# Kernel tuning notes

Measured on AMD Instinct MI355X. Metric: run time of the kernel, lower is better.

## Reference

```python
import jax, jax.numpy as jnp
import numpy as np

B, D_IN, H, OUT = 65536, 3072, 100, 10
CUTOFF = 0.5


def setup_inputs() -> dict:
    key = jax.random.key(0)
    ks = jax.random.split(key, 7)
    x = jax.random.normal(ks[0], (B, D_IN), jnp.float32)
    # Kaiming-ish scaling so activations stay sane through 15 relu layers
    w_in = jax.random.normal(ks[1], (D_IN, H), jnp.float32) * np.float32(1.0 / np.sqrt(D_IN))
    b_in = jax.random.normal(ks[2], (H,), jnp.float32) * np.float32(0.01)
    w_hid = jax.random.normal(ks[3], (14, H, H), jnp.float32) * np.float32(1.0 / np.sqrt(H))
    b_hid = jax.random.normal(ks[4], (14, H), jnp.float32) * np.float32(0.01)
    w_out = jax.random.normal(ks[5], (3, H, OUT), jnp.float32) * np.float32(1.0 / np.sqrt(H))
    b_out = jax.random.normal(ks[6], (3, OUT), jnp.float32) * np.float32(0.01)
    return {"x": x, "w_in": w_in, "b_in": b_in, "w_hid": w_hid, "b_hid": b_hid, "w_out": w_out, "b_out": b_out}


def reference(x, w_in, b_in, w_hid, b_hid, w_out, b_out):
    # Stage 0 (net0): first layer D_IN->H then 4 hidden layers H->H, all relu
    h = jax.nn.relu(x @ w_in + b_in)
    for i in range(0, 4):
        h = jax.nn.relu(h @ w_hid[i] + b_hid[i])
    out0 = h @ w_out[0] + b_out[0]                     # [B, 10]
    conf0 = jnp.max(out0, axis=1) > CUTOFF             # cutoff_mask

    # Stage 1 (net1): 5 hidden layers H->H on net0's hidden features
    for i in range(4, 9):
        h = jax.nn.relu(h @ w_hid[i] + b_hid[i])
    out1 = h @ w_out[1] + b_out[1]
    conf1 = jnp.max(out1, axis=1) > CUTOFF

    # Stage 2 (net2): 5 hidden layers H->H, output registered unconditionally
    for i in range(9, 14):
        h = jax.nn.relu(h @ w_hid[i] + b_hid[i])
    out2 = h @ w_out[2] + b_out[2]

    # Filter/reordered_output: each sample takes the output of the first stage
    # at which it was confident (early-exit cascade, dense-masked equivalent).
    final = jnp.where(conf0[:, None], out0, jnp.where(conf1[:, None], out1, out2))
    return final
```

## Files before the change

kernel.cpp:

```cpp
#include <hip/hip_runtime.h>


typedef __fp16 h2   __attribute__((ext_vector_type(2)));
typedef __fp16 h8v  __attribute__((ext_vector_type(8)));
typedef float  f4v  __attribute__((ext_vector_type(4)));
typedef float  f16v __attribute__((ext_vector_type(16)));

#define CHUNK 16384

static constexpr unsigned OFF_W1  = 0;
static constexpr unsigned OFF_WH  = 96u * CHUNK;
static constexpr unsigned OFF_WO  = OFF_WH + 56u * CHUNK;
static constexpr unsigned OFF_BIN = OFF_WO + 3u * CHUNK;
static constexpr unsigned OFF_H1  = OFF_BIN + 512;

__device__ __forceinline__ unsigned bc2(h2 v) { return __builtin_bit_cast(unsigned, v); }

__device__ __forceinline__ f4v ntld4(const float* p) {
  return __builtin_nontemporal_load((const f4v*)p);
}

__device__ __forceinline__ void lds_cp16(const char* g, char* l) {
  __builtin_amdgcn_global_load_lds(
      (const __attribute__((address_space(1))) void*)g,
      (__attribute__((address_space(3))) void*)l, 16, 0, 0);
}

__device__ __forceinline__ void stage1(const char* g, char* l, int tid) {
  lds_cp16(g + tid * 16, l + tid * 16);
}
__device__ __forceinline__ void stage2(const char* g, char* l, int tid) {
  lds_cp16(g + tid * 16, l + tid * 16);
  lds_cp16(g + 8192 + tid * 16, l + 8192 + tid * 16);
}

__device__ __forceinline__ void cvt8(f4v a, f4v b, h8v& hi, h8v& lo) {
  h2 h0 = __builtin_amdgcn_cvt_pkrtz(a[0], a[1]);
  h2 h1 = __builtin_amdgcn_cvt_pkrtz(a[2], a[3]);
  h2 h2_ = __builtin_amdgcn_cvt_pkrtz(b[0], b[1]);
  h2 h3 = __builtin_amdgcn_cvt_pkrtz(b[2], b[3]);
  h2 l0 = __builtin_amdgcn_cvt_pkrtz(a[0] - (float)h0[0], a[1] - (float)h0[1]);
  h2 l1 = __builtin_amdgcn_cvt_pkrtz(a[2] - (float)h1[0], a[3] - (float)h1[1]);
  h2 l2 = __builtin_amdgcn_cvt_pkrtz(b[0] - (float)h2_[0], b[1] - (float)h2_[1]);
  h2 l3 = __builtin_amdgcn_cvt_pkrtz(b[2] - (float)h3[0], b[3] - (float)h3[1]);
  hi = h8v{h0[0], h0[1], h1[0], h1[1], h2_[0], h2_[1], h3[0], h3[1]};
  lo = h8v{l0[0], l0[1], l1[0], l1[1], l2[0], l2[1], l3[0], l3[1]};
}

__device__ __forceinline__ void split4s(f4v v, uint2& hi, uint2& lo) {
  h2 a = __builtin_amdgcn_cvt_pkrtz(v[0], v[1]);
  h2 b = __builtin_amdgcn_cvt_pkrtz(v[2], v[3]);
  h2 c = __builtin_amdgcn_cvt_pkrtz(v[0] - (float)a[0], v[1] - (float)a[1]);
  h2 d = __builtin_amdgcn_cvt_pkrtz(v[2] - (float)b[0], v[3] - (float)b[1]);
  hi = make_uint2(bc2(a), bc2(b));
  lo = make_uint2(bc2(c), bc2(d));
}

__device__ __forceinline__ void split8w(const float* f, uint4& hi, uint4& lo) {
  h2 h0 = __builtin_amdgcn_cvt_pkrtz(f[0], f[1]);
  h2 h1 = __builtin_amdgcn_cvt_pkrtz(f[2], f[3]);
  h2 h2_ = __builtin_amdgcn_cvt_pkrtz(f[4], f[5]);
  h2 h3 = __builtin_amdgcn_cvt_pkrtz(f[6], f[7]);
  h2 l0 = __builtin_amdgcn_cvt_pkrtz(f[0] - (float)h0[0], f[1] - (float)h0[1]);
  h2 l1 = __builtin_amdgcn_cvt_pkrtz(f[2] - (float)h1[0], f[3] - (float)h1[1]);
  h2 l2 = __builtin_amdgcn_cvt_pkrtz(f[4] - (float)h2_[0], f[5] - (float)h2_[1]);
  h2 l3 = __builtin_amdgcn_cvt_pkrtz(f[6] - (float)h3[0], f[7] - (float)h3[1]);
  hi = make_uint4(bc2(h0), bc2(h1), bc2(h2_), bc2(h3));
  lo = make_uint4(bc2(l0), bc2(l1), bc2(l2), bc2(l3));
}

__device__ __forceinline__ unsigned item_off(int it) {
  if (it >= 58) return OFF_WO + 2u * CHUNK;
  if (it == 16) return OFF_WO;
  if (it == 37) return OFF_WO + CHUNK;
  int j = it - (it > 16 ? 1 : 0) - (it > 37 ? 1 : 0);
  return OFF_WH + (unsigned)j * CHUNK;
}

__global__ __launch_bounds__(256) void prep_k(
    const float* __restrict__ w_in, const float* __restrict__ b_in,
    const float* __restrict__ w_hid, const float* __restrict__ b_hid,
    const float* __restrict__ w_out, const float* __restrict__ b_out,
    char* __restrict__ ws) {
  int idx = blockIdx.x * 256 + threadIdx.x;
  int lane = idx & 63;
  int grp = idx >> 6;
  float f[8];
  uint4 hi, lo;
  if (grp < 768) {
    int mf = grp & 7, c = grp >> 3;
    int feat = mf * 16 + (lane & 15);
    int g = lane >> 4;
    int kb = c * 32 + g * 4;
#pragma unroll
    for (int e = 0; e < 8; ++e) {
      int k = kb + (e < 4 ? e : 12 + e);
      f[e] = (feat < 100) ? w_in[(size_t)k * 100 + feat] : 0.f;
    }
    split8w(f, hi, lo);
    char* dst = ws + OFF_W1 + (size_t)c * CHUNK + (size_t)mf * 2048 + lane * 16;
    *(uint4*)dst = hi;
    *(uint4*)(dst + 1024) = lo;
    return;
  }
  grp -= 768;
  if (grp < 448) {
    int j = grp & 1, ft = (grp >> 1) & 3, ch = grp >> 3;
    int L = ch >> 2, s = ch & 3;
    int feat = ft * 32 + (lane & 31);
    int k0 = s * 32 + j * 16 + (lane >> 5) * 8;
#pragma unroll
    for (int e = 0; e < 8; ++e) {
      int k = k0 + e;
      float v;
      if (k < 100 && feat < 100)  v = w_hid[(size_t)L * 10000 + k * 100 + feat];
      else if (k == 127)          v = (feat < 100) ? b_hid[L * 100 + feat]
                                                   : (feat == 127 ? 1.f : 0.f);
      else                        v = 0.f;
      f[e] = v;
    }
    split8w(f, hi, lo);
    char* dst = ws + OFF_WH + (size_t)ch * CHUNK + (size_t)((ft * 2 + j) * 2) * 1024 + lane * 16;
    *(uint4*)dst = hi;
    *(uint4*)(dst + 1024) = lo;
    return;
  }
  grp -= 448;
  if (grp < 24) {
    int kb = grp & 7, st = grp >> 3;
    int cls = lane & 31;
    int k0 = kb * 16 + (lane >> 5) * 8;
#pragma unroll
    for (int e = 0; e < 8; ++e) {
      int k = k0 + e;
      float v;
      if (cls < 10 && k < 100) v = w_out[(size_t)st * 1000 + k * 10 + cls];
      else if (k == 127)       v = (cls < 10) ? b_out[st * 10 + cls] : -60000.f;
      else                     v = 0.f;
      f[e] = v;
    }
    split8w(f, hi, lo);
    char* dst = ws + OFF_WO + (size_t)st * CHUNK + (size_t)(kb * 2) * 1024 + lane * 16;
    *(uint4*)dst = hi;
    *(uint4*)(dst + 1024) = lo;
    return;
  }
  grp -= 24;
  if (grp < 2) {
    int i = grp * 64 + lane;
    ((float*)(ws + OFF_BIN))[i] = (i < 100) ? b_in[i] : (i == 127 ? 1.f : 0.f);
  }
}

#define P1_SMEM (3 * CHUNK)

__global__ __launch_bounds__(1024, 4) void p1_k(const float* __restrict__ x,
                                                char* __restrict__ ws) {
  extern __shared__ __align__(16) char sm[];
  const int tid = threadIdx.x;
  const int lane = tid & 63, wid = tid >> 6;
  const int l15 = lane & 15, g = lane >> 4;
  const int tile = blockIdx.x;
  const char* w1g = ws + OFF_W1;
  const float* xr = x + (size_t)(tile * 256 + wid * 16 + l15) * 3072;

  f4v xP[2], xQ[2], xR[2];
  stage1(w1g, sm, tid);
  __builtin_amdgcn_sched_barrier(0);
  xP[0] = ntld4(xr + g * 4);      xP[1] = ntld4(xr + 16 + g * 4);
  __builtin_amdgcn_sched_barrier(0);
  stage1(w1g + CHUNK, sm + CHUNK, tid);
  __builtin_amdgcn_sched_barrier(0);
  xQ[0] = ntld4(xr + 32 + g * 4); xQ[1] = ntld4(xr + 48 + g * 4);
  __builtin_amdgcn_sched_barrier(0);
  xR[0] = ntld4(xr + 64 + g * 4); xR[1] = ntld4(xr + 80 + g * 4);
  __builtin_amdgcn_sched_barrier(0);

  f4v acc[8] = {};
  const int abase = lane * 16;

  auto step = [&](int s, f4v (&xa)[2]) {
    if (s <= 93)      asm volatile("s_waitcnt vmcnt(5)" ::: "memory");
    else if (s == 94) asm volatile("s_waitcnt vmcnt(3)" ::: "memory");
    else              asm volatile("s_waitcnt vmcnt(0)" ::: "memory");
    __builtin_amdgcn_s_barrier();
    asm volatile("" ::: "memory");

    h8v bhi, blo;
    cvt8(xa[0], xa[1], bhi, blo);
    if (s + 2 < 96) stage1(w1g + (size_t)(s + 2) * CHUNK, sm + ((s + 2) % 3) * CHUNK, tid);
    __builtin_amdgcn_sched_barrier(0);
    if (s + 3 < 96) {
      const int o = (s + 3) * 32 + g * 4;
      xa[0] = ntld4(xr + o); xa[1] = ntld4(xr + o + 16);
    }
    __builtin_amdgcn_sched_barrier(0);

    const char* ab = sm + (s % 3) * CHUNK + abase;
#pragma unroll
    for (int mf = 0; mf < 8; ++mf) {
      h8v ahi = *(const h8v*)(ab + mf * 2048);
      h8v alo = *(const h8v*)(ab + mf * 2048 + 1024);
      acc[mf] = __builtin_amdgcn_mfma_f32_16x16x32_f16(ahi, bhi, acc[mf], 0, 0, 0);
      acc[mf] = __builtin_amdgcn_mfma_f32_16x16x32_f16(ahi, blo, acc[mf], 0, 0, 0);
      acc[mf] = __builtin_amdgcn_mfma_f32_16x16x32_f16(alo, bhi, acc[mf], 0, 0, 0);
    }
  };

#pragma unroll 1
  for (int s3 = 0; s3 < 96; s3 += 3) {
    step(s3, xP);
    step(s3 + 1, xQ);
    step(s3 + 2, xR);
  }

  const float* bp = (const float*)(ws + OFF_BIN);
  const int p2tile = tile * 2 + (wid >> 3);
  const int rt = (wid >> 1) & 3;
  const int l31 = (wid & 1) * 16 + l15;
  char* hb = ws + OFF_H1 + (size_t)p2tile * 65536;
#pragma unroll
  for (int mf = 0; mf < 8; ++mf) {
    f4v bi = *(const f4v*)(bp + mf * 16 + g * 4);
    f4v v = acc[mf] + bi;
    v[0] = fmaxf(v[0], 0.f); v[1] = fmaxf(v[1], 0.f);
    v[2] = fmaxf(v[2], 0.f); v[3] = fmaxf(v[3], 0.f);
    uint2 hi, lo;
    split4s(v, hi, lo);
    char* dst = hb + (size_t)(rt * 8 + mf) * 2048 + (g >> 1) * 512 + l31 * 16 + (g & 1) * 8;
    *(uint2*)dst = hi;
    *(uint2*)(dst + 1024) = lo;
  }
}

#define P2_SMEM (65536 + 3 * CHUNK)

__global__ __launch_bounds__(512, 2) void p2_k(char* __restrict__ ws,
                                               float* __restrict__ out) {
  extern __shared__ __align__(16) char sm[];
  char* hsm = sm;
  char* wsm = sm + 65536;
  const int tid = threadIdx.x;
  const int lane = tid & 63, wid = tid >> 6;
  const int mr = wid & 1, rt = wid >> 1;
  const int l31 = lane & 31, gg = lane >> 5;
  const int tile = blockIdx.x;

  {
    const char* hg = ws + OFF_H1 + (size_t)tile * 65536;
#pragma unroll
    for (int i = 0; i < 8; ++i)
      lds_cp16(hg + i * 8192 + tid * 16, hsm + i * 8192 + tid * 16);
    __builtin_amdgcn_sched_barrier(0);
    stage2(ws + item_off(0), wsm, tid);
    stage2(ws + item_off(1), wsm + CHUNK, tid);
  }

  const f16v z16 = {};
  f16v a0 = {}, a1 = {};
  float s0[6], s1[6], s2[6];
  bool c0 = false, c1 = false;

  auto ring_top = [&](int i) {
    asm volatile("s_waitcnt vmcnt(2)" ::: "memory");
    __builtin_amdgcn_s_barrier();
    asm volatile("" ::: "memory");
    stage2(ws + item_off(i + 2), wsm + ((i + 2) % 3) * CHUNK, tid);
  };

  auto hidden = [&](int base) {
#pragma unroll
    for (int ss = 0; ss < 4; ++ss) {
      ring_top(base + ss);
      const char* wb = wsm + ((base + ss) % 3) * CHUNK + lane * 16;
      const char* hbp = hsm + rt * 16384 + ss * 4096 + lane * 16;
      h8v bh0 = *(const h8v*)(hbp);
      h8v bl0 = *(const h8v*)(hbp + 1024);
      h8v bh1 = *(const h8v*)(hbp + 2048);
      h8v bl1 = *(const h8v*)(hbp + 3072);
      const char* ab0 = wb + (mr * 2) * 4096;
      const char* ab1 = ab0 + 4096;
      h8v ah, al;
      ah = *(const h8v*)(ab0);        al = *(const h8v*)(ab0 + 1024);
      a0 = __builtin_amdgcn_mfma_f32_32x32x16_f16(ah, bh0, a0, 0, 0, 0);
      a0 = __builtin_amdgcn_mfma_f32_32x32x16_f16(ah, bl0, a0, 0, 0, 0);
      a0 = __builtin_amdgcn_mfma_f32_32x32x16_f16(al, bh0, a0, 0, 0, 0);
      ah = *(const h8v*)(ab0 + 2048); al = *(const h8v*)(ab0 + 3072);
      a0 = __builtin_amdgcn_mfma_f32_32x32x16_f16(ah, bh1, a0, 0, 0, 0);
      a0 = __builtin_amdgcn_mfma_f32_32x32x16_f16(ah, bl1, a0, 0, 0, 0);
      a0 = __builtin_amdgcn_mfma_f32_32x32x16_f16(al, bh1, a0, 0, 0, 0);
      ah = *(const h8v*)(ab1);        al = *(const h8v*)(ab1 + 1024);
      a1 = __builtin_amdgcn_mfma_f32_32x32x16_f16(ah, bh0, a1, 0, 0, 0);
      a1 = __builtin_amdgcn_mfma_f32_32x32x16_f16(ah, bl0, a1, 0, 0, 0);
      a1 = __builtin_amdgcn_mfma_f32_32x32x16_f16(al, bh0, a1, 0, 0, 0);
      ah = *(const h8v*)(ab1 + 2048); al = *(const h8v*)(ab1 + 3072);
      a1 = __builtin_amdgcn_mfma_f32_32x32x16_f16(ah, bh1, a1, 0, 0, 0);
      a1 = __builtin_amdgcn_mfma_f32_32x32x16_f16(ah, bl1, a1, 0, 0, 0);
      a1 = __builtin_amdgcn_mfma_f32_32x32x16_f16(al, bh1, a1, 0, 0, 0);
    }
    __builtin_amdgcn_s_barrier();
    asm volatile("" ::: "memory");
#pragma unroll
    for (int fi = 0; fi < 2; ++fi) {
      const int ftb = mr * 2 + fi;
#pragma unroll
      for (int q = 0; q < 4; ++q) {
        f4v v = fi ? f4v{a1[4 * q], a1[4 * q + 1], a1[4 * q + 2], a1[4 * q + 3]}
                   : f4v{a0[4 * q], a0[4 * q + 1], a0[4 * q + 2], a0[4 * q + 3]};
        v[0] = fmaxf(v[0], 0.f); v[1] = fmaxf(v[1], 0.f);
        v[2] = fmaxf(v[2], 0.f); v[3] = fmaxf(v[3], 0.f);
        uint2 hi, lo;
        split4s(v, hi, lo);
        const int kblk = ftb * 2 + (q >> 1);
        char* dst = hsm + (size_t)((rt * 8 + kblk) * 2) * 1024 + ((q & 1) * 32 + l31) * 16 + gg * 8;
        *(uint2*)dst = hi;
        *(uint2*)(dst + 1024) = lo;
      }
    }
    asm volatile("s_waitcnt lgkmcnt(0)" ::: "memory");
    __builtin_amdgcn_s_barrier();
    asm volatile("" ::: "memory");
    a0 = z16;
    a1 = z16;
  };

  auto wstage = [&](int i, float (&sv)[6], bool* cb) {
    ring_top(i);
    const char* wb = wsm + (i % 3) * CHUNK + lane * 16;
    if (mr == 0) {
      f16v oa = {};
#pragma unroll
      for (int kb = 0; kb < 8; ++kb) {
        h8v ah = *(const h8v*)(wb + kb * 2048);
        h8v al = *(const h8v*)(wb + kb * 2048 + 1024);
        const char* hbp = hsm + rt * 16384 + kb * 2048 + lane * 16;
        h8v bh = *(const h8v*)(hbp);
        h8v bl = *(const h8v*)(hbp + 1024);
        oa = __builtin_amdgcn_mfma_f32_32x32x16_f16(ah, bh, oa, 0, 0, 0);
        oa = __builtin_amdgcn_mfma_f32_32x32x16_f16(ah, bl, oa, 0, 0, 0);
        oa = __builtin_amdgcn_mfma_f32_32x32x16_f16(al, bh, oa, 0, 0, 0);
      }
      float m = oa[0];
#pragma unroll
      for (int r = 1; r < 16; ++r) m = fmaxf(m, oa[r]);
      m = fmaxf(m, __shfl_xor(m, 32, 64));
      if (cb) *cb = (m > 0.5f);
      sv[0] = oa[0]; sv[1] = oa[1]; sv[2] = oa[2];
      sv[3] = oa[3]; sv[4] = oa[4]; sv[5] = oa[5];
    }
  };

  hidden(0); hidden(4); hidden(8); hidden(12);
  wstage(16, s0, &c0);
  hidden(17); hidden(21); hidden(25); hidden(29); hidden(33);
  wstage(37, s1, &c1);
  hidden(38); hidden(42); hidden(46); hidden(50); hidden(54);
  wstage(58, s2, nullptr);

  if (mr == 0) {
    float r[6];
#pragma unroll
    for (int j = 0; j < 6; ++j) r[j] = c0 ? s0[j] : (c1 ? s1[j] : s2[j]);
    float* dp = out + (size_t)(tile * 128 + rt * 32 + l31) * 10;
    if (gg == 0) {
      *(float2*)(dp)     = make_float2(r[0], r[1]);
      *(float2*)(dp + 2) = make_float2(r[2], r[3]);
      *(float2*)(dp + 8) = make_float2(r[4], r[5]);
    } else {
      *(float2*)(dp + 4) = make_float2(r[0], r[1]);
      *(float2*)(dp + 6) = make_float2(r[2], r[3]);
    }
  }
}

extern "C" void kernel_launch(void* const* d_in, const int* in_sizes, int n_in,
                              void* d_out, int out_size, void* d_ws, size_t ws_size,
                              hipStream_t stream) {
  (void)in_sizes; (void)n_in; (void)out_size; (void)ws_size;
  const float* x     = (const float*)d_in[0];
  const float* w_in  = (const float*)d_in[1];
  const float* b_in  = (const float*)d_in[2];
  const float* w_hid = (const float*)d_in[3];
  const float* b_hid = (const float*)d_in[4];
  const float* w_out = (const float*)d_in[5];
  const float* b_out = (const float*)d_in[6];
  float* out = (float*)d_out;
  char* ws = (char*)d_ws;

  (void)hipFuncSetAttribute((const void*)p1_k,
                            hipFuncAttributeMaxDynamicSharedMemorySize, P1_SMEM);
  (void)hipFuncSetAttribute((const void*)p2_k,
                            hipFuncAttributeMaxDynamicSharedMemorySize, P2_SMEM);

  prep_k<<<311, 256, 0, stream>>>(w_in, b_in, w_hid, b_hid, w_out, b_out, ws);
  p1_k<<<256, 1024, P1_SMEM, stream>>>(x, ws);
  p2_k<<<512, 512, P2_SMEM, stream>>>(ws, out);
}
```

Baseline: 307.4 us.

## Double K-step size in first-layer GEMM and deepen hidden-layer weight ring to four

```diff
diff --git a/kernel.cpp b/kernel.cpp
--- a/kernel.cpp
+++ b/kernel.cpp
@@ -26,8 +26,9 @@
       (__attribute__((address_space(3))) void*)l, 16, 0, 0);
 }
 
-__device__ __forceinline__ void stage1(const char* g, char* l, int tid) {
+__device__ __forceinline__ void stageW(const char* g, char* l, int tid) {
   lds_cp16(g + tid * 16, l + tid * 16);
+  lds_cp16(g + 16384 + tid * 16, l + 16384 + tid * 16);
 }
 __device__ __forceinline__ void stage2(const char* g, char* l, int tid) {
   lds_cp16(g + tid * 16, l + tid * 16);
@@ -152,7 +153,7 @@
   }
 }
 
-#define P1_SMEM (3 * CHUNK)
+#define P1_SMEM (3 * 32768)
 
 __global__ __launch_bounds__(1024, 4) void p1_k(const float* __restrict__ x,
                                                 char* __restrict__ ws) {
@@ -164,54 +165,67 @@
   const char* w1g = ws + OFF_W1;
   const float* xr = x + (size_t)(tile * 256 + wid * 16 + l15) * 3072;
 
-  f4v xP[2], xQ[2], xR[2];
-  stage1(w1g, sm, tid);
+  f4v xP[4], xQ[4];
+  stageW(w1g, sm, tid);
   __builtin_amdgcn_sched_barrier(0);
-  xP[0] = ntld4(xr + g * 4);      xP[1] = ntld4(xr + 16 + g * 4);
+  {
+    const int o = g * 4;
+    xP[0] = ntld4(xr + o);      xP[1] = ntld4(xr + o + 16);
+    xP[2] = ntld4(xr + o + 32); xP[3] = ntld4(xr + o + 48);
+  }
   __builtin_amdgcn_sched_barrier(0);
-  stage1(w1g + CHUNK, sm + CHUNK, tid);
+  stageW(w1g + 2 * CHUNK, sm + 32768, tid);
   __builtin_amdgcn_sched_barrier(0);
-  xQ[0] = ntld4(xr + 32 + g * 4); xQ[1] = ntld4(xr + 48 + g * 4);
-  __builtin_amdgcn_sched_barrier(0);
-  xR[0] = ntld4(xr + 64 + g * 4); xR[1] = ntld4(xr + 80 + g * 4);
+  {
+    const int o = 64 + g * 4;
+    xQ[0] = ntld4(xr + o);      xQ[1] = ntld4(xr + o + 16);
+    xQ[2] = ntld4(xr + o + 32); xQ[3] = ntld4(xr + o + 48);
+  }
   __builtin_amdgcn_sched_barrier(0);
 
   f4v acc[8] = {};
   const int abase = lane * 16;
 
-  auto step = [&](int s, f4v (&xa)[2]) {
-    if (s <= 93)      asm volatile("s_waitcnt vmcnt(5)" ::: "memory");
-    else if (s == 94) asm volatile("s_waitcnt vmcnt(3)" ::: "memory");
-    else              asm volatile("s_waitcnt vmcnt(0)" ::: "memory");
+  auto step = [&](int s, f4v (&xa)[4]) {
+    if (s == 47) asm volatile("s_waitcnt vmcnt(0)" ::: "memory");
+    else         asm volatile("s_waitcnt vmcnt(6)" ::: "memory");
     __builtin_amdgcn_s_barrier();
     asm volatile("" ::: "memory");
 
-    h8v bhi, blo;
-    cvt8(xa[0], xa[1], bhi, blo);
-    if (s + 2 < 96) stage1(w1g + (size_t)(s + 2) * CHUNK, sm + ((s + 2) % 3) * CHUNK, tid);
+    h8v bh0, bl0, bh1, bl1;
+    cvt8(xa[0], xa[1], bh0, bl0);
+    cvt8(xa[2], xa[3], bh1, bl1);
+    if (s + 2 < 48) {
+      stageW(w1g + (size_t)(2 * s + 4) * CHUNK, sm + ((s + 2) % 3) * 32768, tid);
+    }
     __builtin_amdgcn_sched_barrier(0);
-    if (s + 3 < 96) {
-      const int o = (s + 3) * 32 + g * 4;
-      xa[0] = ntld4(xr + o); xa[1] = ntld4(xr + o + 16);
+    if (s + 2 < 48) {
+      const int o = (s + 2) * 64 + g * 4;
+      xa[0] = ntld4(xr + o);      xa[1] = ntld4(xr + o + 16);
+      xa[2] = ntld4(xr + o + 32); xa[3] = ntld4(xr + o + 48);
     }
     __builtin_amdgcn_sched_barrier(0);
 
-    const char* ab = sm + (s % 3) * CHUNK + abase;
+    const char* ab = sm + (s % 3) * 32768 + abase;
 #pragma unroll
     for (int mf = 0; mf < 8; ++mf) {
       h8v ahi = *(const h8v*)(ab + mf * 2048);
       h8v alo = *(const h8v*)(ab + mf * 2048 + 1024);
-      acc[mf] = __builtin_amdgcn_mfma_f32_16x16x32_f16(ahi, bhi, acc[mf], 0, 0, 0);
-      acc[mf] = __builtin_amdgcn_mfma_f32_16x16x32_f16(ahi, blo, acc[mf], 0, 0, 0);
-      acc[mf] = __builtin_amdgcn_mfma_f32_16x16x32_f16(alo, bhi, acc[mf], 0, 0, 0);
+      acc[mf] = __builtin_amdgcn_mfma_f32_16x16x32_f16(ahi, bh0, acc[mf], 0, 0, 0);
+      acc[mf] = __builtin_amdgcn_mfma_f32_16x16x32_f16(ahi, bl0, acc[mf], 0, 0, 0);
+      acc[mf] = __builtin_amdgcn_mfma_f32_16x16x32_f16(alo, bh0, acc[mf], 0, 0, 0);
+      h8v ahiB = *(const h8v*)(ab + 16384 + mf * 2048);
+      h8v aloB = *(const h8v*)(ab + 16384 + mf * 2048 + 1024);
+      acc[mf] = __builtin_amdgcn_mfma_f32_16x16x32_f16(ahiB, bh1, acc[mf], 0, 0, 0);
+      acc[mf] = __builtin_amdgcn_mfma_f32_16x16x32_f16(ahiB, bl1, acc[mf], 0, 0, 0);
+      acc[mf] = __builtin_amdgcn_mfma_f32_16x16x32_f16(aloB, bh1, acc[mf], 0, 0, 0);
     }
   };
 
 #pragma unroll 1
-  for (int s3 = 0; s3 < 96; s3 += 3) {
-    step(s3, xP);
-    step(s3 + 1, xQ);
-    step(s3 + 2, xR);
+  for (int s2 = 0; s2 < 48; s2 += 2) {
+    step(s2, xP);
+    step(s2 + 1, xQ);
   }
 
   const float* bp = (const float*)(ws + OFF_BIN);
@@ -233,7 +247,7 @@
   }
 }
 
-#define P2_SMEM (65536 + 3 * CHUNK)
+#define P2_SMEM (65536 + 4 * CHUNK)
 
 __global__ __launch_bounds__(512, 2) void p2_k(char* __restrict__ ws,
                                                float* __restrict__ out) {
@@ -254,6 +268,7 @@
     __builtin_amdgcn_sched_barrier(0);
     stage2(ws + item_off(0), wsm, tid);
     stage2(ws + item_off(1), wsm + CHUNK, tid);
+    stage2(ws + item_off(2), wsm + 2 * CHUNK, tid);
   }
 
   const f16v z16 = {};
@@ -262,17 +277,17 @@
   bool c0 = false, c1 = false;
 
   auto ring_top = [&](int i) {
-    asm volatile("s_waitcnt vmcnt(2)" ::: "memory");
+    asm volatile("s_waitcnt vmcnt(4)" ::: "memory");
     __builtin_amdgcn_s_barrier();
     asm volatile("" ::: "memory");
-    stage2(ws + item_off(i + 2), wsm + ((i + 2) % 3) * CHUNK, tid);
+    stage2(ws + item_off(i + 3), wsm + ((i + 3) & 3) * CHUNK, tid);
   };
 
   auto hidden = [&](int base) {
 #pragma unroll
     for (int ss = 0; ss < 4; ++ss) {
       ring_top(base + ss);
-      const char* wb = wsm + ((base + ss) % 3) * CHUNK + lane * 16;
+      const char* wb = wsm + ((base + ss) & 3) * CHUNK + lane * 16;
       const char* hbp = hsm + rt * 16384 + ss * 4096 + lane * 16;
       h8v bh0 = *(const h8v*)(hbp);
       h8v bl0 = *(const h8v*)(hbp + 1024);
@@ -326,7 +341,7 @@
 
   auto wstage = [&](int i, float (&sv)[6], bool* cb) {
     ring_top(i);
-    const char* wb = wsm + (i % 3) * CHUNK + lane * 16;
+    const char* wb = wsm + (i & 3) * CHUNK + lane * 16;
     if (mr == 0) {
       f16v oa = {};
 #pragma unroll
```

New measurement: 308.3 us. About the same (+0.3%).

## Store first-layer weights as single fp16 and deepen second-kernel weight ring

Applied to the files above, without the earlier changes.

```diff
diff --git a/kernel.cpp b/kernel.cpp
--- a/kernel.cpp
+++ b/kernel.cpp
@@ -6,10 +6,11 @@
 typedef float  f4v  __attribute__((ext_vector_type(4)));
 typedef float  f16v __attribute__((ext_vector_type(16)));
 
+#define W1CH  8192
 #define CHUNK 16384
 
 static constexpr unsigned OFF_W1  = 0;
-static constexpr unsigned OFF_WH  = 96u * CHUNK;
+static constexpr unsigned OFF_WH  = 96u * W1CH;
 static constexpr unsigned OFF_WO  = OFF_WH + 56u * CHUNK;
 static constexpr unsigned OFF_BIN = OFF_WO + 3u * CHUNK;
 static constexpr unsigned OFF_H1  = OFF_BIN + 512;
@@ -26,9 +27,6 @@
       (__attribute__((address_space(3))) void*)l, 16, 0, 0);
 }
 
-__device__ __forceinline__ void stage1(const char* g, char* l, int tid) {
-  lds_cp16(g + tid * 16, l + tid * 16);
-}
 __device__ __forceinline__ void stage2(const char* g, char* l, int tid) {
   lds_cp16(g + tid * 16, l + tid * 16);
   lds_cp16(g + 8192 + tid * 16, l + 8192 + tid * 16);
@@ -92,15 +90,16 @@
     int feat = mf * 16 + (lane & 15);
     int g = lane >> 4;
     int kb = c * 32 + g * 4;
+    __fp16 hf[8];
 #pragma unroll
     for (int e = 0; e < 8; ++e) {
       int k = kb + (e < 4 ? e : 12 + e);
-      f[e] = (feat < 100) ? w_in[(size_t)k * 100 + feat] : 0.f;
-    }
-    split8w(f, hi, lo);
-    char* dst = ws + OFF_W1 + (size_t)c * CHUNK + (size_t)mf * 2048 + lane * 16;
-    *(uint4*)dst = hi;
-    *(uint4*)(dst + 1024) = lo;
+      hf[e] = (__fp16)((feat < 100) ? w_in[(size_t)k * 100 + feat] : 0.f);
+    }
+    uint4 w = make_uint4(bc2(h2{hf[0], hf[1]}), bc2(h2{hf[2], hf[3]}),
+                         bc2(h2{hf[4], hf[5]}), bc2(h2{hf[6], hf[7]}));
+    char* dst = ws + OFF_W1 + (size_t)c * W1CH + (size_t)mf * 1024 + lane * 16;
+    *(uint4*)dst = w;
     return;
   }
   grp -= 768;
@@ -152,7 +151,7 @@
   }
 }
 
-#define P1_SMEM (3 * CHUNK)
+#define P1_SMEM (3 * 16384)
 
 __global__ __launch_bounds__(1024, 4) void p1_k(const float* __restrict__ x,
                                                 char* __restrict__ ws) {
@@ -164,46 +163,49 @@
   const char* w1g = ws + OFF_W1;
   const float* xr = x + (size_t)(tile * 256 + wid * 16 + l15) * 3072;
 
+  auto stW = [&](int t) {
+    lds_cp16(w1g + (size_t)t * 16384 + tid * 16, sm + (t % 3) * 16384 + tid * 16);
+  };
+
   f4v xP[2], xQ[2], xR[2];
-  stage1(w1g, sm, tid);
+  auto ldx = [&](int s, f4v (&xa)[2]) {
+    const int o = s * 32 + g * 4;
+    xa[0] = ntld4(xr + o); xa[1] = ntld4(xr + o + 16);
+  };
+
+  stW(0);
   __builtin_amdgcn_sched_barrier(0);
-  xP[0] = ntld4(xr + g * 4);      xP[1] = ntld4(xr + 16 + g * 4);
+  ldx(0, xP);
   __builtin_amdgcn_sched_barrier(0);
-  stage1(w1g + CHUNK, sm + CHUNK, tid);
+  ldx(1, xQ);
   __builtin_amdgcn_sched_barrier(0);
-  xQ[0] = ntld4(xr + 32 + g * 4); xQ[1] = ntld4(xr + 48 + g * 4);
+  stW(1);
   __builtin_amdgcn_sched_barrier(0);
-  xR[0] = ntld4(xr + 64 + g * 4); xR[1] = ntld4(xr + 80 + g * 4);
+  ldx(2, xR);
   __builtin_amdgcn_sched_barrier(0);
 
   f4v acc[8] = {};
-  const int abase = lane * 16;
 
   auto step = [&](int s, f4v (&xa)[2]) {
     if (s <= 93)      asm volatile("s_waitcnt vmcnt(5)" ::: "memory");
-    else if (s == 94) asm volatile("s_waitcnt vmcnt(3)" ::: "memory");
+    else if (s == 94) asm volatile("s_waitcnt vmcnt(2)" ::: "memory");
     else              asm volatile("s_waitcnt vmcnt(0)" ::: "memory");
     __builtin_amdgcn_s_barrier();
     asm volatile("" ::: "memory");
 
-    h8v bhi, blo;
-    cvt8(xa[0], xa[1], bhi, blo);
-    if (s + 2 < 96) stage1(w1g + (size_t)(s + 2) * CHUNK, sm + ((s + 2) % 3) * CHUNK, tid);
+    h8v bh, bl;
+    cvt8(xa[0], xa[1], bh, bl);
+    if ((s & 1) && (s + 3 < 96)) stW((s + 3) >> 1);
     __builtin_amdgcn_sched_barrier(0);
-    if (s + 3 < 96) {
-      const int o = (s + 3) * 32 + g * 4;
-      xa[0] = ntld4(xr + o); xa[1] = ntld4(xr + o + 16);
-    }
+    if (s + 3 < 96) ldx(s + 3, xa);
     __builtin_amdgcn_sched_barrier(0);
 
-    const char* ab = sm + (s % 3) * CHUNK + abase;
+    const char* ab = sm + ((s >> 1) % 3) * 16384 + (s & 1) * 8192 + lane * 16;
 #pragma unroll
     for (int mf = 0; mf < 8; ++mf) {
-      h8v ahi = *(const h8v*)(ab + mf * 2048);
-      h8v alo = *(const h8v*)(ab + mf * 2048 + 1024);
-      acc[mf] = __builtin_amdgcn_mfma_f32_16x16x32_f16(ahi, bhi, acc[mf], 0, 0, 0);
-      acc[mf] = __builtin_amdgcn_mfma_f32_16x16x32_f16(ahi, blo, acc[mf], 0, 0, 0);
-      acc[mf] = __builtin_amdgcn_mfma_f32_16x16x32_f16(alo, bhi, acc[mf], 0, 0, 0);
+      h8v a = *(const h8v*)(ab + mf * 1024);
+      acc[mf] = __builtin_amdgcn_mfma_f32_16x16x32_f16(a, bh, acc[mf], 0, 0, 0);
+      acc[mf] = __builtin_amdgcn_mfma_f32_16x16x32_f16(a, bl, acc[mf], 0, 0, 0);
     }
   };
 
@@ -233,7 +235,7 @@
   }
 }
 
-#define P2_SMEM (65536 + 3 * CHUNK)
+#define P2_SMEM (65536 + 4 * CHUNK)
 
 __global__ __launch_bounds__(512, 2) void p2_k(char* __restrict__ ws,
                                                float* __restrict__ out) {
@@ -254,6 +256,7 @@
     __builtin_amdgcn_sched_barrier(0);
     stage2(ws + item_off(0), wsm, tid);
     stage2(ws + item_off(1), wsm + CHUNK, tid);
+    stage2(ws + item_off(2), wsm + 2 * CHUNK, tid);
   }
 
   const f16v z16 = {};
@@ -262,17 +265,17 @@
   bool c0 = false, c1 = false;
 
   auto ring_top = [&](int i) {
-    asm volatile("s_waitcnt vmcnt(2)" ::: "memory");
+    asm volatile("s_waitcnt vmcnt(4)" ::: "memory");
     __builtin_amdgcn_s_barrier();
     asm volatile("" ::: "memory");
-    stage2(ws + item_off(i + 2), wsm + ((i + 2) % 3) * CHUNK, tid);
+    stage2(ws + item_off(i + 3), wsm + ((i + 3) & 3) * CHUNK, tid);
   };
 
   auto hidden = [&](int base) {
 #pragma unroll
     for (int ss = 0; ss < 4; ++ss) {
       ring_top(base + ss);
-      const char* wb = wsm + ((base + ss) % 3) * CHUNK + lane * 16;
+      const char* wb = wsm + ((base + ss) & 3) * CHUNK + lane * 16;
       const char* hbp = hsm + rt * 16384 + ss * 4096 + lane * 16;
       h8v bh0 = *(const h8v*)(hbp);
       h8v bl0 = *(const h8v*)(hbp + 1024);
@@ -326,7 +329,7 @@
 
   auto wstage = [&](int i, float (&sv)[6], bool* cb) {
     ring_top(i);
-    const char* wb = wsm + (i % 3) * CHUNK + lane * 16;
+    const char* wb = wsm + (i & 3) * CHUNK + lane * 16;
     if (mr == 0) {
       f16v oa = {};
 #pragma unroll
```

New measurement: 295.6 us. -3.8%, faster.
